# Optimization experiments

Hardware: AMD Instinct MI355X
Metric: run time of the kernel (lower is better)

The kernel has to match this reference:

```python
import jax, jax.numpy as jnp
import numpy as np

N, E, IN_DIM, HID, HEADS, LAT = 50000, 800000, 128, 32, 4, 32


def _gat_params(key, fin, heads, cout):
    k1, k2, k3 = jax.random.split(key, 3)
    s = 1.0 / np.sqrt(fin)
    W = jax.random.uniform(k1, (fin, heads * cout), minval=-s, maxval=s, dtype=jnp.float32)
    a_src = jax.random.normal(k2, (heads, cout), dtype=jnp.float32) * 0.1
    a_dst = jax.random.normal(k3, (heads, cout), dtype=jnp.float32) * 0.1
    b = jnp.zeros((heads * cout,), dtype=jnp.float32)
    return W, a_src, a_dst, b


def setup_inputs() -> dict:
    key = jax.random.key(0)
    ks = jax.random.split(key, 8)
    x = jax.random.normal(ks[0], (N, IN_DIM), dtype=jnp.float32)
    edge_index = jax.random.randint(ks[1], (2, E), 0, N, dtype=jnp.int64)
    W1, a1s, a1d, b1 = _gat_params(ks[2], IN_DIM, HEADS, HID)
    W2, a2s, a2d, b2 = _gat_params(ks[3], HID * HEADS, HEADS, HID)
    Wl, als, ald, bl = _gat_params(ks[4], HID * HEADS, 1, LAT)
    Wd, ads_, add_, bd = _gat_params(ks[5], LAT, 1, HID)
    sdec = 1.0 / np.sqrt(HID)
    Wdec = jax.random.uniform(ks[6], (HID, IN_DIM), minval=-sdec, maxval=sdec, dtype=jnp.float32)
    bdec = jnp.zeros((IN_DIM,), dtype=jnp.float32)
    return {"x": x, "edge_index": edge_index,
            "W1": W1, "a1s": a1s, "a1d": a1d, "b1": b1,
            "W2": W2, "a2s": a2s, "a2d": a2d, "b2": b2,
            "Wl": Wl, "als": als, "ald": ald, "bl": bl,
            "Wd": Wd, "ads": ads_, "add": add_, "bd": bd,
            "Wdec": Wdec, "bdec": bdec}


def gat_conv(x, src, dst, W, a_s, a_d, b, n, concat=True):
    """PyG-style GATConv (eval mode, self-loops already in src/dst)."""
    H, C = a_s.shape
    h = (x @ W).reshape(n, H, C)                      # [N,H,C]
    alpha_src = jnp.sum(h * a_s, axis=-1)             # [N,H]
    alpha_dst = jnp.sum(h * a_d, axis=-1)             # [N,H]
    e = jax.nn.leaky_relu(alpha_src[src] + alpha_dst[dst], 0.2)  # [E,H]
    m = jax.ops.segment_max(e, dst, num_segments=n)
    m = jnp.where(jnp.isfinite(m), m, 0.0)
    ex = jnp.exp(e - m[dst])
    denom = jax.ops.segment_sum(ex, dst, num_segments=n)
    coef = ex / (denom[dst] + 1e-16)                  # [E,H]
    out = jax.ops.segment_sum(coef[:, :, None] * h[src], dst, num_segments=n)  # [N,H,C]
    out = out.reshape(n, H * C) if concat else out.mean(axis=1)
    return out + b


def reference(x, edge_index, W1, a1s, a1d, b1, W2, a2s, a2d, b2,
              Wl, als, ald, bl, Wd, ads, add, bd, Wdec, bdec):
    n = x.shape[0]
    # add self-loops (PyG GATConv default)
    loops = jnp.arange(n, dtype=edge_index.dtype)
    src = jnp.concatenate([edge_index[0], loops])
    dst = jnp.concatenate([edge_index[1], loops])
    lrelu = lambda v: jax.nn.leaky_relu(v, 0.01)
    x1 = lrelu(gat_conv(x, src, dst, W1, a1s, a1d, b1, n))
    x2 = lrelu(gat_conv(x1, src, dst, W2, a2s, a2d, b2, n))
    z = gat_conv(x2, src, dst, Wl, als, ald, bl, n)
    xr = lrelu(gat_conv(z, src, dst, Wd, ads, add, bd, n))
    reconstructed = xr @ Wdec + bdec + x
    return reconstructed, z
```

## Files before the change

### kernel.cpp

```cpp
#include <hip/hip_runtime.h>
#include <math.h>

#define CAP 64

typedef __attribute__((ext_vector_type(8))) short short8;
typedef __attribute__((ext_vector_type(4))) float f32x4;

__device__ __forceinline__ float lrelu02(float v) { return v > 0.f ? v : 0.2f * v; }
__device__ __forceinline__ float lrelu01(float v) { return v > 0.f ? v : 0.01f * v; }

__device__ __forceinline__ float bfl(unsigned u) { return __uint_as_float(u << 16); }
__device__ __forceinline__ float bfh(unsigned u) { return __uint_as_float(u & 0xffff0000u); }
__device__ __forceinline__ unsigned short f2bf(float f) {
  unsigned u = __float_as_uint(f);
  return (unsigned short)((u + 0x7fffu + ((u >> 16) & 1u)) >> 16);
}
__device__ __forceinline__ unsigned pk2bf(float lo, float hi) {
  return (unsigned)f2bf(lo) | ((unsigned)f2bf(hi) << 16);
}

__global__ __launch_bounds__(256) void fill_k(const int* __restrict__ ei, int* __restrict__ deg,
                                              unsigned short* __restrict__ cols, int E, int nr, int Nn) {
  const int r = blockIdx.x & 7;
  const int c = blockIdx.x >> 3;
  const unsigned lo = (unsigned)(r * nr);
  const unsigned hi = (unsigned)min(Nn, (r + 1) * nr);
  const int chunk = (E + 255) >> 8;
  const int e0 = c * chunk;
  const int e1 = min(E, e0 + chunk);
  for (int e = e0 + (int)threadIdx.x; e < e1; e += 256) {
    unsigned d = (unsigned)ei[E + e];
    if (d >= lo && d < hi) {
      int s = ei[e];
      int pos = atomicAdd(&deg[d], 1);
      if (pos < CAP) cols[(size_t)d * CAP + pos] = (unsigned short)s;
    }
  }
}

__global__ __launch_bounds__(256) void cvtw_k(const float* __restrict__ W1, const float* __restrict__ W2,
                                              const float* __restrict__ Wl, const float* __restrict__ Wd,
                                              const float* __restrict__ Wdec,
                                              unsigned short* __restrict__ t1, unsigned short* __restrict__ t2,
                                              unsigned short* __restrict__ tl, unsigned short* __restrict__ td,
                                              unsigned short* __restrict__ tdec) {
  int b = blockIdx.x, tid = threadIdx.x;
  const float* src; unsigned short* dst; int K, NC, base;
  if (b < 64)       { src = W1;   dst = t1;   K = 128; NC = 128; base = 0; }
  else if (b < 128) { src = W2;   dst = t2;   K = 128; NC = 128; base = 64; }
  else if (b < 144) { src = Wl;   dst = tl;   K = 128; NC = 32;  base = 128; }
  else if (b < 148) { src = Wd;   dst = td;   K = 32;  NC = 32;  base = 144; }
  else              { src = Wdec; dst = tdec; K = 32;  NC = 128; base = 148; }
  int e = (b - base) * 256 + tid;
  if (e < K * NC) {
    int k = e / NC, c = e - k * NC;
    dst[c * K + k] = f2bf(src[e]);
  }
}

template<int K, int NC, bool OUT16, bool ALPHA, bool RB, bool IN32>
__global__ __launch_bounds__(256) void gemm_mfma(const void* __restrict__ Av,
                                                 const unsigned short* __restrict__ Wt,
                                                 const float* __restrict__ bias,
                                                 const float* __restrict__ resid,
                                                 void* __restrict__ Cv,
                                                 const float* __restrict__ a_s, const float* __restrict__ a_d,
                                                 float* __restrict__ asrc, float* __restrict__ adst, int M) {
  constexpr int BM = (NC == 128) ? 64 : 128;
  constexpr int NKS = K / 32;
  constexpr int RS = (NC == 128) ? 4 : 2;
  constexpr int SWZ = (K == 128) ? 7 : 3;
  constexpr int CH = BM * K / 2048;
  __shared__ unsigned short At[BM * K];
  const int tid = threadIdx.x;
  const int wid = tid >> 6, lane = tid & 63;
  const int g = lane >> 4, l15 = lane & 15;
  const int row0 = blockIdx.x * BM;

  short8 wf[NKS][2];
  const int cglob0 = ((NC == 128) ? 32 * wid : 0) + l15;
#pragma unroll
  for (int ks = 0; ks < NKS; ++ks)
#pragma unroll
    for (int cf = 0; cf < 2; ++cf)
      wf[ks][cf] = *(const short8*)(Wt + (size_t)(cglob0 + 16 * cf) * K + ks * 32 + g * 8);

  uint4 ra[CH];
  if constexpr (IN32) {
    const float* Af = (const float*)Av;
#pragma unroll
    for (int c = 0; c < CH; ++c) {
      int ch = c * 256 + tid;
      int row = ch * 8 / K;
      int col = ch * 8 - row * K;
      float4 lo = {0.f, 0.f, 0.f, 0.f}, hi = {0.f, 0.f, 0.f, 0.f};
      if (row0 + row < M) {
        lo = *(const float4*)(Af + (size_t)(row0 + row) * K + col);
        hi = *(const float4*)(Af + (size_t)(row0 + row) * K + col + 4);
      }
      ra[c] = make_uint4(pk2bf(lo.x, lo.y), pk2bf(lo.z, lo.w), pk2bf(hi.x, hi.y), pk2bf(hi.z, hi.w));
    }
  } else {
    const unsigned short* Ab = (const unsigned short*)Av;
#pragma unroll
    for (int c = 0; c < CH; ++c) {
      int ch = c * 256 + tid;
      int row = ch * 8 / K;
      ra[c] = (row0 + row < M) ? *(const uint4*)(Ab + (size_t)row0 * K + ch * 8)
                               : make_uint4(0u, 0u, 0u, 0u);
    }
  }
#pragma unroll
  for (int c = 0; c < CH; ++c) {
    int ch = c * 256 + tid;
    int row = ch * 8 / K;
    int off = ch * 16 - row * (2 * K);
    *(uint4*)((char*)At + row * (2 * K) + (off ^ ((row & SWZ) << 4))) = ra[c];
  }
  __syncthreads();

  f32x4 acc[RS][2];
#pragma unroll
  for (int r = 0; r < RS; ++r)
#pragma unroll
    for (int cf = 0; cf < 2; ++cf) acc[r][cf] = (f32x4){0.f, 0.f, 0.f, 0.f};

  const int rwave = (NC == 128) ? 0 : 32 * wid;
#pragma unroll
  for (int ks = 0; ks < NKS; ++ks) {
#pragma unroll
    for (int r = 0; r < RS; ++r) {
      int row = rwave + 16 * r + l15;
      int off = ks * 64 + g * 16;
      short8 af = *(const short8*)((const char*)At + row * (2 * K) + (off ^ ((row & SWZ) << 4)));
#pragma unroll
      for (int cf = 0; cf < 2; ++cf)
        acc[r][cf] = __builtin_amdgcn_mfma_f32_16x16x32_bf16(wf[ks][cf], af, acc[r][cf], 0, 0, 0);
    }
  }

#pragma unroll
  for (int r = 0; r < RS; ++r) {
    const int row = row0 + rwave + 16 * r + l15;
    const bool ok = row < M;
#pragma unroll
    for (int cf = 0; cf < 2; ++cf) {
      const int colbase = ((NC == 128) ? 32 * wid : 0) + 16 * cf + 4 * g;
      if constexpr (OUT16) {
        if (ok) {
          unsigned short* Cb = (unsigned short*)Cv;
          ushort4 o;
          o.x = f2bf(acc[r][cf][0]); o.y = f2bf(acc[r][cf][1]);
          o.z = f2bf(acc[r][cf][2]); o.w = f2bf(acc[r][cf][3]);
          *(ushort4*)(Cb + (size_t)row * NC + colbase) = o;
        }
      } else if constexpr (RB) {
        if (ok) {
          float* C = (float*)Cv;
          float4 bi = *(const float4*)(bias + colbase);
          float4 rv = *(const float4*)(resid + (size_t)row * NC + colbase);
          float4 o;
          o.x = acc[r][cf][0] + bi.x + rv.x;
          o.y = acc[r][cf][1] + bi.y + rv.y;
          o.z = acc[r][cf][2] + bi.z + rv.z;
          o.w = acc[r][cf][3] + bi.w + rv.w;
          *(float4*)(C + (size_t)row * NC + colbase) = o;
        }
      }
    }
    if constexpr (ALPHA) {
      constexpr int H = NC / 32;
      const int head = (NC == 128) ? wid : 0;
      float ps = 0.f, pd = 0.f;
#pragma unroll
      for (int cf = 0; cf < 2; ++cf) {
        float4 sa = *(const float4*)(a_s + head * 32 + 16 * cf + 4 * g);
        float4 da = *(const float4*)(a_d + head * 32 + 16 * cf + 4 * g);
        ps += acc[r][cf][0] * sa.x + acc[r][cf][1] * sa.y + acc[r][cf][2] * sa.z + acc[r][cf][3] * sa.w;
        pd += acc[r][cf][0] * da.x + acc[r][cf][1] * da.y + acc[r][cf][2] * da.z + acc[r][cf][3] * da.w;
      }
      ps += __shfl_xor(ps, 16, 64); pd += __shfl_xor(pd, 16, 64);
      ps += __shfl_xor(ps, 32, 64); pd += __shfl_xor(pd, 32, 64);
      if (g == 0 && ok) {
        asrc[(size_t)row * H + head] = ps;
        adst[(size_t)row * H + head] = pd;
      }
    }
  }
}

template<int ACT>
__global__ __launch_bounds__(256) void agg128_k(const unsigned short* __restrict__ Hb,
                                                const float* __restrict__ asrc,
                                                const float* __restrict__ adst,
                                                const int* __restrict__ deg,
                                                const unsigned short* __restrict__ cols,
                                                const float* __restrict__ bias,
                                                unsigned short* __restrict__ Y, int Nn) {
  __shared__ float wl[4][256];
  __shared__ int sl[4][64];
  const int wid = threadIdx.x >> 6, lane = threadIdx.x & 63;
  const int node = blockIdx.x * 4 + wid;
  if (node >= Nn) return;
  const int eidx = lane >> 2, h4 = lane & 3;
  const float adr = adst[node * 4 + h4];
  const float asr = asrc[node * 4 + h4];
  int cnt = deg[node];
  cnt = cnt > CAP ? CAP : cnt;
  const unsigned short* __restrict__ cl = cols + (size_t)node * CAP;
  float dn = 0.f;
  for (int c0 = 0; c0 < cnt; c0 += 16) {
    int e = c0 + eidx;
    bool valid = e < cnt;
    int s = valid ? (int)cl[e] : 0;
    float w = valid ? __expf(lrelu02(asrc[s * 4 + h4] + adr)) : 0.f;
    wl[wid][e * 4 + h4] = w;
    if (h4 == 0) sl[wid][e] = s * 16;
    dn += w;
  }
  dn += __shfl_xor(dn, 4, 64);
  dn += __shfl_xor(dn, 8, 64);
  dn += __shfl_xor(dn, 16, 64);
  dn += __shfl_xor(dn, 32, 64);
  float wself = __expf(lrelu02(asr + adr));
  dn += wself;
  float inv = 1.f / (dn + 1e-16f);
  float wsinv = wself * inv;
  for (int j = lane; j < cnt * 4; j += 64) wl[wid][j] *= inv;
  float wns = __shfl(wsinv, (lane & 15) >> 2, 64);
  __builtin_amdgcn_wave_barrier();

  const uint4* __restrict__ HB = (const uint4*)Hb;
  const int sub = lane >> 4;
  const int c8 = lane & 15;
  const int h = c8 >> 2;
  float a0 = 0.f, a1 = 0.f, a2 = 0.f, a3 = 0.f, a4 = 0.f, a5 = 0.f, a6 = 0.f, a7 = 0.f;
  float p0 = 0.f, p1 = 0.f, p2 = 0.f, p3 = 0.f, p4 = 0.f, p5 = 0.f, p6 = 0.f, p7 = 0.f;
  int i = sub;
  for (; i + 4 < cnt; i += 8) {
    int o0 = sl[wid][i];
    int o1 = sl[wid][i + 4];
    float w0 = wl[wid][i * 4 + h];
    float w1 = wl[wid][(i + 4) * 4 + h];
    uint4 u0 = HB[o0 + c8];
    uint4 u1 = HB[o1 + c8];
    a0 += w0 * bfl(u0.x); a1 += w0 * bfh(u0.x); a2 += w0 * bfl(u0.y); a3 += w0 * bfh(u0.y);
    a4 += w0 * bfl(u0.z); a5 += w0 * bfh(u0.z); a6 += w0 * bfl(u0.w); a7 += w0 * bfh(u0.w);
    p0 += w1 * bfl(u1.x); p1 += w1 * bfh(u1.x); p2 += w1 * bfl(u1.y); p3 += w1 * bfh(u1.y);
    p4 += w1 * bfl(u1.z); p5 += w1 * bfh(u1.z); p6 += w1 * bfl(u1.w); p7 += w1 * bfh(u1.w);
  }
  for (; i < cnt; i += 4) {
    int o0 = sl[wid][i];
    float w0 = wl[wid][i * 4 + h];
    uint4 u0 = HB[o0 + c8];
    a0 += w0 * bfl(u0.x); a1 += w0 * bfh(u0.x); a2 += w0 * bfl(u0.y); a3 += w0 * bfh(u0.y);
    a4 += w0 * bfl(u0.z); a5 += w0 * bfh(u0.z); a6 += w0 * bfl(u0.w); a7 += w0 * bfh(u0.w);
  }
  a0 += p0; a1 += p1; a2 += p2; a3 += p3; a4 += p4; a5 += p5; a6 += p6; a7 += p7;
#pragma unroll
  for (int off = 16; off <= 32; off <<= 1) {
    a0 += __shfl_xor(a0, off, 64); a1 += __shfl_xor(a1, off, 64);
    a2 += __shfl_xor(a2, off, 64); a3 += __shfl_xor(a3, off, 64);
    a4 += __shfl_xor(a4, off, 64); a5 += __shfl_xor(a5, off, 64);
    a6 += __shfl_xor(a6, off, 64); a7 += __shfl_xor(a7, off, 64);
  }
  if (lane < 16) {
    uint4 us = HB[node * 16 + c8];
    float4 b0 = *(const float4*)(bias + c8 * 8);
    float4 b1 = *(const float4*)(bias + c8 * 8 + 4);
    float o0 = a0 + wns * bfl(us.x) + b0.x;
    float o1 = a1 + wns * bfh(us.x) + b0.y;
    float o2 = a2 + wns * bfl(us.y) + b0.z;
    float o3 = a3 + wns * bfh(us.y) + b0.w;
    float o4 = a4 + wns * bfl(us.z) + b1.x;
    float o5 = a5 + wns * bfh(us.z) + b1.y;
    float o6 = a6 + wns * bfl(us.w) + b1.z;
    float o7 = a7 + wns * bfh(us.w) + b1.w;
    if (ACT == 1) {
      o0 = lrelu01(o0); o1 = lrelu01(o1); o2 = lrelu01(o2); o3 = lrelu01(o3);
      o4 = lrelu01(o4); o5 = lrelu01(o5); o6 = lrelu01(o6); o7 = lrelu01(o7);
    }
    ((uint4*)Y)[(size_t)node * 16 + c8] =
        make_uint4(pk2bf(o0, o1), pk2bf(o2, o3), pk2bf(o4, o5), pk2bf(o6, o7));
  }
}

template<int ACT, int OMODE>
__global__ __launch_bounds__(256) void agg32_k(const unsigned short* __restrict__ Hb,
                                               const float* __restrict__ asrc, const float* __restrict__ adst,
                                               const int* __restrict__ deg,
                                               const unsigned short* __restrict__ cols,
                                               const float* __restrict__ bias, void* __restrict__ Yv,
                                               void* __restrict__ Yv2, int Nn) {
  __shared__ float wl[4][64];
  __shared__ int sl[4][64];
  const int wid = threadIdx.x >> 6, lane = threadIdx.x & 63;
  const int node = blockIdx.x * 4 + wid;
  if (node >= Nn) return;
  const float adr = adst[node], asr = asrc[node];
  int cnt = deg[node];
  cnt = cnt > CAP ? CAP : cnt;
  const unsigned short* __restrict__ cl = cols + (size_t)node * CAP;
  int s = (lane < cnt) ? (int)cl[lane] : 0;
  float w = (lane < cnt) ? __expf(lrelu02(asrc[s] + adr)) : 0.f;
  float dn = w;
#pragma unroll
  for (int off = 32; off >= 1; off >>= 1) dn += __shfl_xor(dn, off, 64);
  float ws = __expf(lrelu02(asr + adr));
  dn += ws;
  float inv = 1.f / (dn + 1e-16f);
  wl[wid][lane] = w * inv;
  sl[wid][lane] = s * 8;
  __builtin_amdgcn_wave_barrier();

  const uint2* __restrict__ HB = (const uint2*)Hb;
  const int sub = lane >> 3;
  const int c = lane & 7;
  float a0 = 0.f, a1 = 0.f, a2 = 0.f, a3 = 0.f;
  float p0 = 0.f, p1 = 0.f, p2 = 0.f, p3 = 0.f;
  int i = sub;
  for (; i + 8 < cnt; i += 16) {
    int o0 = sl[wid][i];
    int o1 = sl[wid][i + 8];
    float w0 = wl[wid][i];
    float w1 = wl[wid][i + 8];
    uint2 u0 = HB[o0 + c];
    uint2 u1 = HB[o1 + c];
    a0 += w0 * bfl(u0.x); a1 += w0 * bfh(u0.x); a2 += w0 * bfl(u0.y); a3 += w0 * bfh(u0.y);
    p0 += w1 * bfl(u1.x); p1 += w1 * bfh(u1.x); p2 += w1 * bfl(u1.y); p3 += w1 * bfh(u1.y);
  }
  for (; i < cnt; i += 8) {
    int o0 = sl[wid][i];
    float w0 = wl[wid][i];
    uint2 u0 = HB[o0 + c];
    a0 += w0 * bfl(u0.x); a1 += w0 * bfh(u0.x); a2 += w0 * bfl(u0.y); a3 += w0 * bfh(u0.y);
  }
  a0 += p0; a1 += p1; a2 += p2; a3 += p3;
#pragma unroll
  for (int off = 8; off <= 32; off <<= 1) {
    a0 += __shfl_xor(a0, off, 64); a1 += __shfl_xor(a1, off, 64);
    a2 += __shfl_xor(a2, off, 64); a3 += __shfl_xor(a3, off, 64);
  }
  if (lane < 8) {
    uint2 us = HB[node * 8 + c];
    float wns = ws * inv;
    float4 bb = ((const float4*)bias)[c];
    float o0 = a0 + wns * bfl(us.x) + bb.x;
    float o1 = a1 + wns * bfh(us.x) + bb.y;
    float o2 = a2 + wns * bfl(us.y) + bb.z;
    float o3 = a3 + wns * bfh(us.y) + bb.w;
    if (ACT == 1) { o0 = lrelu01(o0); o1 = lrelu01(o1); o2 = lrelu01(o2); o3 = lrelu01(o3); }
    if constexpr (OMODE == 2) {
      ((float4*)Yv)[(size_t)node * 8 + c] = make_float4(o0, o1, o2, o3);
      ((uint2*)Yv2)[(size_t)node * 8 + c] = make_uint2(pk2bf(o0, o1), pk2bf(o2, o3));
    } else {
      ((uint2*)Yv)[(size_t)node * 8 + c] = make_uint2(pk2bf(o0, o1), pk2bf(o2, o3));
    }
  }
}

extern "C" void kernel_launch(void* const* d_in, const int* in_sizes, int n_in,
                              void* d_out, int out_size, void* d_ws, size_t ws_size,
                              hipStream_t stream) {
  const float* x = (const float*)d_in[0];
  const int* ei = (const int*)d_in[1];
  const float* W1 = (const float*)d_in[2];
  const float* a1s = (const float*)d_in[3];
  const float* a1d = (const float*)d_in[4];
  const float* b1 = (const float*)d_in[5];
  const float* W2 = (const float*)d_in[6];
  const float* a2s = (const float*)d_in[7];
  const float* a2d = (const float*)d_in[8];
  const float* b2 = (const float*)d_in[9];
  const float* Wl = (const float*)d_in[10];
  const float* als = (const float*)d_in[11];
  const float* ald = (const float*)d_in[12];
  const float* bl = (const float*)d_in[13];
  const float* Wd = (const float*)d_in[14];
  const float* ads = (const float*)d_in[15];
  const float* add_ = (const float*)d_in[16];
  const float* bd = (const float*)d_in[17];
  const float* Wdec = (const float*)d_in[18];
  const float* bdec = (const float*)d_in[19];

  const int N = in_sizes[0] / 128;
  const int E = in_sizes[1] / 2;
  const int nr = (N + 7) / 8;

  char* ws = (char*)d_ws;
  auto alloc = [&](size_t bytes) {
    char* p = ws;
    ws += (bytes + 255) & ~(size_t)255;
    return p;
  };
  unsigned short* cols = (unsigned short*)alloc((size_t)N * CAP * 2);
  int* deg = (int*)alloc((size_t)N * 4);
  unsigned short* hb16 = (unsigned short*)alloc((size_t)N * 128 * 2);
  float* asrc = (float*)alloc((size_t)N * 4 * 4);
  float* adst = (float*)alloc((size_t)N * 4 * 4);
  unsigned short* x12 = (unsigned short*)alloc((size_t)N * 128 * 2);
  unsigned short* z16 = (unsigned short*)alloc((size_t)N * 32 * 2);
  unsigned short* xr16 = (unsigned short*)alloc((size_t)N * 32 * 2);
  unsigned short* W1t = (unsigned short*)alloc(128 * 128 * 2);
  unsigned short* W2t = (unsigned short*)alloc(128 * 128 * 2);
  unsigned short* Wlt = (unsigned short*)alloc(128 * 32 * 2);
  unsigned short* Wdt = (unsigned short*)alloc(32 * 32 * 2);
  unsigned short* Wdect = (unsigned short*)alloc(32 * 128 * 2);

  float* rec = (float*)d_out;
  float* zout = (float*)d_out + (size_t)N * 128;

  hipMemsetAsync(deg, 0, (size_t)N * 4, stream);
  fill_k<<<2048, 256, 0, stream>>>(ei, deg, cols, E, nr, N);
  cvtw_k<<<164, 256, 0, stream>>>(W1, W2, Wl, Wd, Wdec, W1t, W2t, Wlt, Wdt, Wdect);

  const int gG128 = (N + 63) / 64;
  const int gG32 = (N + 127) / 128;
  const int gAg = (N + 3) / 4;

  gemm_mfma<128, 128, true, true, false, true><<<gG128, 256, 0, stream>>>(
      x, W1t, nullptr, nullptr, hb16, a1s, a1d, asrc, adst, N);
  agg128_k<1><<<gAg, 256, 0, stream>>>(hb16, asrc, adst, deg, cols, b1, x12, N);

  gemm_mfma<128, 128, true, true, false, false><<<gG128, 256, 0, stream>>>(
      x12, W2t, nullptr, nullptr, hb16, a2s, a2d, asrc, adst, N);
  agg128_k<1><<<gAg, 256, 0, stream>>>(hb16, asrc, adst, deg, cols, b2, x12, N);

  gemm_mfma<128, 32, true, true, false, false><<<gG32, 256, 0, stream>>>(
      x12, Wlt, nullptr, nullptr, hb16, als, ald, asrc, adst, N);
  agg32_k<0, 2><<<gAg, 256, 0, stream>>>(hb16, asrc, adst, deg, cols, bl, zout, z16, N);

  gemm_mfma<32, 32, true, true, false, false><<<gG32, 256, 0, stream>>>(
      z16, Wdt, nullptr, nullptr, hb16, ads, add_, asrc, adst, N);
  agg32_k<1, 1><<<gAg, 256, 0, stream>>>(hb16, asrc, adst, deg, cols, bd, xr16, nullptr, N);

  gemm_mfma<32, 128, false, false, true, false><<<gG128, 256, 0, stream>>>(
      xr16, Wdect, bdec, x, rec, nullptr, nullptr, nullptr, nullptr, N);
}
```

Before: 324.9 us.

## Fuse small decoder GEMMs into the aggregation epilogues and merge prep kernels

The 32x32 decoder projection (plus its attention logits) is now computed inside the layer-3 aggregation kernel, and the 32x128 reconstruction GEMM with bias and residual runs inside the layer-4 aggregation kernel. The edge-bucketing and weight-conversion kernels are merged into one launch. This drops two GEMM launches and the z16/xr16 intermediate round trips through global memory. In exchange, each aggregation block stages 4 KB or 16 KB of fp32 weights in LDS, and the small matmuls run as scalar FMA loops per wave instead of on MFMA.

```diff
diff --git a/kernel.cpp b/kernel.cpp
--- a/kernel.cpp
+++ b/kernel.cpp
@@ -19,57 +19,52 @@
   return (unsigned)f2bf(lo) | ((unsigned)f2bf(hi) << 16);
 }
 
-__global__ __launch_bounds__(256) void fill_k(const int* __restrict__ ei, int* __restrict__ deg,
-                                              unsigned short* __restrict__ cols, int E, int nr, int Nn) {
-  const int r = blockIdx.x & 7;
-  const int c = blockIdx.x >> 3;
-  const unsigned lo = (unsigned)(r * nr);
-  const unsigned hi = (unsigned)min(Nn, (r + 1) * nr);
-  const int chunk = (E + 255) >> 8;
-  const int e0 = c * chunk;
-  const int e1 = min(E, e0 + chunk);
-  for (int e = e0 + (int)threadIdx.x; e < e1; e += 256) {
-    unsigned d = (unsigned)ei[E + e];
-    if (d >= lo && d < hi) {
-      int s = ei[e];
-      int pos = atomicAdd(&deg[d], 1);
-      if (pos < CAP) cols[(size_t)d * CAP + pos] = (unsigned short)s;
-    }
-  }
-}
-
-__global__ __launch_bounds__(256) void cvtw_k(const float* __restrict__ W1, const float* __restrict__ W2,
-                                              const float* __restrict__ Wl, const float* __restrict__ Wd,
-                                              const float* __restrict__ Wdec,
+__global__ __launch_bounds__(256) void prep_k(const int* __restrict__ ei, int* __restrict__ deg,
+                                              unsigned short* __restrict__ cols, int E, int nr, int Nn,
+                                              const float* __restrict__ W1, const float* __restrict__ W2,
+                                              const float* __restrict__ Wl,
                                               unsigned short* __restrict__ t1, unsigned short* __restrict__ t2,
-                                              unsigned short* __restrict__ tl, unsigned short* __restrict__ td,
-                                              unsigned short* __restrict__ tdec) {
-  int b = blockIdx.x, tid = threadIdx.x;
-  const float* src; unsigned short* dst; int K, NC, base;
-  if (b < 64)       { src = W1;   dst = t1;   K = 128; NC = 128; base = 0; }
-  else if (b < 128) { src = W2;   dst = t2;   K = 128; NC = 128; base = 64; }
-  else if (b < 144) { src = Wl;   dst = tl;   K = 128; NC = 32;  base = 128; }
-  else if (b < 148) { src = Wd;   dst = td;   K = 32;  NC = 32;  base = 144; }
-  else              { src = Wdec; dst = tdec; K = 32;  NC = 128; base = 148; }
-  int e = (b - base) * 256 + tid;
-  if (e < K * NC) {
-    int k = e / NC, c = e - k * NC;
-    dst[c * K + k] = f2bf(src[e]);
-  }
-}
-
-template<int K, int NC, bool OUT16, bool ALPHA, bool RB, bool IN32>
+                                              unsigned short* __restrict__ tl) {
+  if (blockIdx.x < 2048) {
+    const int r = blockIdx.x & 7;
+    const int c = blockIdx.x >> 3;
+    const unsigned lo = (unsigned)(r * nr);
+    const unsigned hi = (unsigned)min(Nn, (r + 1) * nr);
+    const int chunk = (E + 255) >> 8;
+    const int e0 = c * chunk;
+    const int e1 = min(E, e0 + chunk);
+    for (int e = e0 + (int)threadIdx.x; e < e1; e += 256) {
+      unsigned d = (unsigned)ei[E + e];
+      if (d >= lo && d < hi) {
+        int s = ei[e];
+        int pos = atomicAdd(&deg[d], 1);
+        if (pos < CAP) cols[(size_t)d * CAP + pos] = (unsigned short)s;
+      }
+    }
+  } else {
+    int b = blockIdx.x - 2048, tid = threadIdx.x;
+    const float* src; unsigned short* dst; int K, NC, base;
+    if (b < 64)       { src = W1; dst = t1; K = 128; NC = 128; base = 0; }
+    else if (b < 128) { src = W2; dst = t2; K = 128; NC = 128; base = 64; }
+    else              { src = Wl; dst = tl; K = 128; NC = 32;  base = 128; }
+    int e = (b - base) * 256 + tid;
+    if (e < K * NC) {
+      int k = e / NC, c2 = e - k * NC;
+      dst[c2 * K + k] = f2bf(src[e]);
+    }
+  }
+}
+
+template<int K, int NC, bool ALPHA, bool IN32>
 __global__ __launch_bounds__(256) void gemm_mfma(const void* __restrict__ Av,
                                                  const unsigned short* __restrict__ Wt,
-                                                 const float* __restrict__ bias,
-                                                 const float* __restrict__ resid,
-                                                 void* __restrict__ Cv,
+                                                 unsigned short* __restrict__ Cb,
                                                  const float* __restrict__ a_s, const float* __restrict__ a_d,
                                                  float* __restrict__ asrc, float* __restrict__ adst, int M) {
   constexpr int BM = (NC == 128) ? 64 : 128;
   constexpr int NKS = K / 32;
   constexpr int RS = (NC == 128) ? 4 : 2;
-  constexpr int SWZ = (K == 128) ? 7 : 3;
+  constexpr int SWZ = 7;
   constexpr int CH = BM * K / 2048;
   __shared__ unsigned short At[BM * K];
   const int tid = threadIdx.x;
@@ -146,26 +141,11 @@
 #pragma unroll
     for (int cf = 0; cf < 2; ++cf) {
       const int colbase = ((NC == 128) ? 32 * wid : 0) + 16 * cf + 4 * g;
-      if constexpr (OUT16) {
-        if (ok) {
-          unsigned short* Cb = (unsigned short*)Cv;
-          ushort4 o;
-          o.x = f2bf(acc[r][cf][0]); o.y = f2bf(acc[r][cf][1]);
-          o.z = f2bf(acc[r][cf][2]); o.w = f2bf(acc[r][cf][3]);
-          *(ushort4*)(Cb + (size_t)row * NC + colbase) = o;
-        }
-      } else if constexpr (RB) {
-        if (ok) {
-          float* C = (float*)Cv;
-          float4 bi = *(const float4*)(bias + colbase);
-          float4 rv = *(const float4*)(resid + (size_t)row * NC + colbase);
-          float4 o;
-          o.x = acc[r][cf][0] + bi.x + rv.x;
-          o.y = acc[r][cf][1] + bi.y + rv.y;
-          o.z = acc[r][cf][2] + bi.z + rv.z;
-          o.w = acc[r][cf][3] + bi.w + rv.w;
-          *(float4*)(C + (size_t)row * NC + colbase) = o;
-        }
+      if (ok) {
+        ushort4 o;
+        o.x = f2bf(acc[r][cf][0]); o.y = f2bf(acc[r][cf][1]);
+        o.z = f2bf(acc[r][cf][2]); o.w = f2bf(acc[r][cf][3]);
+        *(ushort4*)(Cb + (size_t)row * NC + colbase) = o;
       }
     }
     if constexpr (ALPHA) {
@@ -285,18 +265,14 @@
   }
 }
 
-template<int ACT, int OMODE>
-__global__ __launch_bounds__(256) void agg32_k(const unsigned short* __restrict__ Hb,
-                                               const float* __restrict__ asrc, const float* __restrict__ adst,
-                                               const int* __restrict__ deg,
-                                               const unsigned short* __restrict__ cols,
-                                               const float* __restrict__ bias, void* __restrict__ Yv,
-                                               void* __restrict__ Yv2, int Nn) {
-  __shared__ float wl[4][64];
-  __shared__ int sl[4][64];
-  const int wid = threadIdx.x >> 6, lane = threadIdx.x & 63;
-  const int node = blockIdx.x * 4 + wid;
-  if (node >= Nn) return;
+template<int ACT>
+__device__ __forceinline__ float4 agg32_core(const unsigned short* __restrict__ Hb,
+                                             const float* __restrict__ asrc, const float* __restrict__ adst,
+                                             const int* __restrict__ deg,
+                                             const unsigned short* __restrict__ cols,
+                                             const float* __restrict__ bias,
+                                             float (*wl)[64], int (*sl)[64],
+                                             int wid, int lane, int node) {
   const float adr = adst[node], asr = asrc[node];
   int cnt = deg[node];
   cnt = cnt > CAP ? CAP : cnt;
@@ -341,22 +317,108 @@
     a0 += __shfl_xor(a0, off, 64); a1 += __shfl_xor(a1, off, 64);
     a2 += __shfl_xor(a2, off, 64); a3 += __shfl_xor(a3, off, 64);
   }
+  float4 out = make_float4(0.f, 0.f, 0.f, 0.f);
   if (lane < 8) {
     uint2 us = HB[node * 8 + c];
     float wns = ws * inv;
     float4 bb = ((const float4*)bias)[c];
-    float o0 = a0 + wns * bfl(us.x) + bb.x;
-    float o1 = a1 + wns * bfh(us.x) + bb.y;
-    float o2 = a2 + wns * bfl(us.y) + bb.z;
-    float o3 = a3 + wns * bfh(us.y) + bb.w;
-    if (ACT == 1) { o0 = lrelu01(o0); o1 = lrelu01(o1); o2 = lrelu01(o2); o3 = lrelu01(o3); }
-    if constexpr (OMODE == 2) {
-      ((float4*)Yv)[(size_t)node * 8 + c] = make_float4(o0, o1, o2, o3);
-      ((uint2*)Yv2)[(size_t)node * 8 + c] = make_uint2(pk2bf(o0, o1), pk2bf(o2, o3));
-    } else {
-      ((uint2*)Yv)[(size_t)node * 8 + c] = make_uint2(pk2bf(o0, o1), pk2bf(o2, o3));
-    }
-  }
+    out.x = a0 + wns * bfl(us.x) + bb.x;
+    out.y = a1 + wns * bfh(us.x) + bb.y;
+    out.z = a2 + wns * bfl(us.y) + bb.z;
+    out.w = a3 + wns * bfh(us.y) + bb.w;
+    if (ACT == 1) { out.x = lrelu01(out.x); out.y = lrelu01(out.y); out.z = lrelu01(out.z); out.w = lrelu01(out.w); }
+  }
+  return out;
+}
+
+__global__ __launch_bounds__(256) void agg32_l3_k(const unsigned short* __restrict__ Hb,
+                                                  const float* __restrict__ asrc, const float* __restrict__ adst,
+                                                  const int* __restrict__ deg,
+                                                  const unsigned short* __restrict__ cols,
+                                                  const float* __restrict__ bl,
+                                                  const float* __restrict__ Wd,
+                                                  const float* __restrict__ ads, const float* __restrict__ add_,
+                                                  float* __restrict__ zout, unsigned short* __restrict__ H4,
+                                                  float* __restrict__ asrcB, float* __restrict__ adstB, int Nn) {
+  __shared__ float Wd_l[32 * 32];
+  __shared__ float wl[4][64];
+  __shared__ int sl[4][64];
+  __shared__ float zb[4][32];
+  {
+    int t = threadIdx.x * 4;
+    *(float4*)&Wd_l[t] = *(const float4*)(Wd + t);
+  }
+  __syncthreads();
+  const int wid = threadIdx.x >> 6, lane = threadIdx.x & 63;
+  const int node = blockIdx.x * 4 + wid;
+  if (node >= Nn) return;
+
+  float4 z = agg32_core<0>(Hb, asrc, adst, deg, cols, bl, wl, sl, wid, lane, node);
+  const int c = lane & 7;
+  if (lane < 8) {
+    ((float4*)zout)[(size_t)node * 8 + c] = z;
+    *(float4*)&zb[wid][c * 4] = z;
+  }
+  __builtin_amdgcn_wave_barrier();
+
+  float h4 = 0.f;
+  const int j = lane & 31;
+#pragma unroll 8
+  for (int k = 0; k < 32; ++k) h4 += zb[wid][k] * Wd_l[k * 32 + j];
+  float ps = 0.f, pd = 0.f;
+  if (lane < 32) {
+    H4[(size_t)node * 32 + j] = f2bf(h4);
+    ps = h4 * ads[j];
+    pd = h4 * add_[j];
+  }
+#pragma unroll
+  for (int off = 1; off <= 16; off <<= 1) { ps += __shfl_xor(ps, off, 64); pd += __shfl_xor(pd, off, 64); }
+  if (lane == 0) {
+    asrcB[node] = ps;
+    adstB[node] = pd;
+  }
+}
+
+__global__ __launch_bounds__(256) void agg32_l4_k(const unsigned short* __restrict__ Hb,
+                                                  const float* __restrict__ asrc, const float* __restrict__ adst,
+                                                  const int* __restrict__ deg,
+                                                  const unsigned short* __restrict__ cols,
+                                                  const float* __restrict__ bd,
+                                                  const float* __restrict__ Wdec,
+                                                  const float* __restrict__ bdec,
+                                                  const float* __restrict__ x,
+                                                  float* __restrict__ rec, int Nn) {
+  __shared__ float Wdec_l[32 * 128];
+  __shared__ float wl[4][64];
+  __shared__ int sl[4][64];
+  __shared__ float xb[4][32];
+  {
+    int t = threadIdx.x * 16;
+#pragma unroll
+    for (int q = 0; q < 4; ++q)
+      *(float4*)&Wdec_l[t + q * 4] = *(const float4*)(Wdec + t + q * 4);
+  }
+  __syncthreads();
+  const int wid = threadIdx.x >> 6, lane = threadIdx.x & 63;
+  const int node = blockIdx.x * 4 + wid;
+  if (node >= Nn) return;
+
+  float4 xr = agg32_core<1>(Hb, asrc, adst, deg, cols, bd, wl, sl, wid, lane, node);
+  const int c = lane & 7;
+  if (lane < 8) *(float4*)&xb[wid][c * 4] = xr;
+  __builtin_amdgcn_wave_barrier();
+
+  float r0 = 0.f, r1 = 0.f;
+#pragma unroll 8
+  for (int k = 0; k < 32; ++k) {
+    float xv = xb[wid][k];
+    r0 += xv * Wdec_l[k * 128 + lane];
+    r1 += xv * Wdec_l[k * 128 + lane + 64];
+  }
+  r0 += bdec[lane] + x[(size_t)node * 128 + lane];
+  r1 += bdec[lane + 64] + x[(size_t)node * 128 + lane + 64];
+  rec[(size_t)node * 128 + lane] = r0;
+  rec[(size_t)node * 128 + lane + 64] = r1;
 }
 
 extern "C" void kernel_launch(void* const* d_in, const int* in_sizes, int n_in,
@@ -398,42 +460,35 @@
   unsigned short* hb16 = (unsigned short*)alloc((size_t)N * 128 * 2);
   float* asrc = (float*)alloc((size_t)N * 4 * 4);
   float* adst = (float*)alloc((size_t)N * 4 * 4);
+  float* asrcB = (float*)alloc((size_t)N * 4);
+  float* adstB = (float*)alloc((size_t)N * 4);
   unsigned short* x12 = (unsigned short*)alloc((size_t)N * 128 * 2);
-  unsigned short* z16 = (unsigned short*)alloc((size_t)N * 32 * 2);
-  unsigned short* xr16 = (unsigned short*)alloc((size_t)N * 32 * 2);
+  unsigned short* hb2 = (unsigned short*)alloc((size_t)N * 32 * 2);
   unsigned short* W1t = (unsigned short*)alloc(128 * 128 * 2);
   unsigned short* W2t = (unsigned short*)alloc(128 * 128 * 2);
   unsigned short* Wlt = (unsigned short*)alloc(128 * 32 * 2);
-  unsigned short* Wdt = (unsigned short*)alloc(32 * 32 * 2);
-  unsigned short* Wdect = (unsigned short*)alloc(32 * 128 * 2);
 
   float* rec = (float*)d_out;
   float* zout = (float*)d_out + (size_t)N * 128;
 
   hipMemsetAsync(deg, 0, (size_t)N * 4, stream);
-  fill_k<<<2048, 256, 0, stream>>>(ei, deg, cols, E, nr, N);
-  cvtw_k<<<164, 256, 0, stream>>>(W1, W2, Wl, Wd, Wdec, W1t, W2t, Wlt, Wdt, Wdect);
+  prep_k<<<2192, 256, 0, stream>>>(ei, deg, cols, E, nr, N, W1, W2, Wl, W1t, W2t, Wlt);
 
   const int gG128 = (N + 63) / 64;
   const int gG32 = (N + 127) / 128;
   const int gAg = (N + 3) / 4;
 
-  gemm_mfma<128, 128, true, true, false, true><<<gG128, 256, 0, stream>>>(
-      x, W1t, nullptr, nullptr, hb16, a1s, a1d, asrc, adst, N);
+  gemm_mfma<128, 128, true, true><<<gG128, 256, 0, stream>>>(
+      x, W1t, hb16, a1s, a1d, asrc, adst, N);
   agg128_k<1><<<gAg, 256, 0, stream>>>(hb16, asrc, adst, deg, cols, b1, x12, N);
 
-  gemm_mfma<128, 128, true, true, false, false><<<gG128, 256, 0, stream>>>(
-      x12, W2t, nullptr, nullptr, hb16, a2s, a2d, asrc, adst, N);
+  gemm_mfma<128, 128, true, false><<<gG128, 256, 0, stream>>>(
+      x12, W2t, hb16, a2s, a2d, asrc, adst, N);
   agg128_k<1><<<gAg, 256, 0, stream>>>(hb16, asrc, adst, deg, cols, b2, x12, N);
 
-  gemm_mfma<128, 32, true, true, false, false><<<gG32, 256, 0, stream>>>(
-      x12, Wlt, nullptr, nullptr, hb16, als, ald, asrc, adst, N);
-  agg32_k<0, 2><<<gAg, 256, 0, stream>>>(hb16, asrc, adst, deg, cols, bl, zout, z16, N);
-
-  gemm_mfma<32, 32, true, true, false, false><<<gG32, 256, 0, stream>>>(
-      z16, Wdt, nullptr, nullptr, hb16, ads, add_, asrc, adst, N);
-  agg32_k<1, 1><<<gAg, 256, 0, stream>>>(hb16, asrc, adst, deg, cols, bd, xr16, nullptr, N);
-
-  gemm_mfma<32, 128, false, false, true, false><<<gG128, 256, 0, stream>>>(
-      xr16, Wdect, bdec, x, rec, nullptr, nullptr, nullptr, nullptr, N);
-}
+  gemm_mfma<128, 32, true, false><<<gG32, 256, 0, stream>>>(
+      x12, Wlt, hb16, als, ald, asrc, adst, N);
+  agg32_l3_k<<<gAg, 256, 0, stream>>>(hb16, asrc, adst, deg, cols, bl, Wd, ads, add_,
+                                      zout, hb2, asrcB, adstB, N);
+  agg32_l4_k<<<gAg, 256, 0, stream>>>(hb2, asrcB, adstB, deg, cols, bd, Wdec, bdec, x, rec, N);
+}
```

Result: slower. 332.5 us (+2.3%).
